# Performance work log

Measured on AMD Instinct MI355X. Metric: run time of the kernel, lower is better.

## Reference

```python
import jax, jax.numpy as jnp
import numpy as np

EPS = 1e-8


def _dtw_distance(cost):
    """Classic DTW DP: D[i,j] = cost[i,j] + min(D[i-1,j], D[i-1,j-1], D[i,j-1]).
    Rows are processed with lax.scan; the within-row left-to-right recurrence
    D[j] = min(a[j], D[j-1] + c[j]) is solved in closed form as a min-plus scan:
    with S = cumsum(c), D = cummin(a - S) + S.
    """
    # first row: only horizontal moves -> running cumsum
    d0 = jnp.cumsum(cost[0])

    def row_step(prev, c):
        # prev: D[i-1, :]  (shape [m]);  c: cost[i, :]
        prev_diag = jnp.concatenate([jnp.full((1,), jnp.inf, prev.dtype), prev[:-1]])
        a = c + jnp.minimum(prev, prev_diag)          # candidate from above / diagonal
        S = jnp.cumsum(c)
        d = jax.lax.cummin(a - S) + S                 # folds in the left-neighbor path
        return d, None

    d_last, _ = jax.lax.scan(row_step, d0, cost[1:])
    return d_last[-1]


def setup_inputs() -> dict:
    key = jax.random.key(0)
    k1, k2 = jax.random.split(key)
    N1, N2, D = 4096, 4096, 1024
    return {
        "trajectory1": jax.random.normal(k1, (N1, D), dtype=jnp.float32),
        "trajectory2": jax.random.normal(k2, (N2, D), dtype=jnp.float32),
    }


def reference(trajectory1, trajectory2):
    # cosine distance matrix: 1 - <t1_hat, t2_hat>
    t1 = trajectory1 / (jnp.linalg.norm(trajectory1, axis=-1, keepdims=True) + EPS)
    t2 = trajectory2 / (jnp.linalg.norm(trajectory2, axis=-1, keepdims=True) + EPS)
    cost = 1.0 - jnp.einsum('id,jd->ij', t1, t2)      # [N1, N2]
    distance = _dtw_distance(cost)
    similarity = 1.0 / (1.0 + distance)
    return similarity
```

## Files before the change

kernel.cpp:

```cpp
#include <hip/hip_runtime.h>
#include <hip/hip_bf16.h>
#include <stdint.h>

#define KDIM 1024
#define NROW 4096
#define NCOL 4096
#define INFV 1e30f
#define INFBITS 0x7149F2CAu
#define BM 128
#define BK 32

#define SKROWS 4160
#define DLAG   28
#define EMAX   360

typedef __bf16 bf16x8 __attribute__((ext_vector_type(8)));
typedef float f32x4 __attribute__((ext_vector_type(4)));

#define CFENCE asm volatile("" ::: "memory")

__device__ __forceinline__ unsigned short f2bf(float f) {
    __hip_bfloat16 h = __float2bfloat16(f);
    return *reinterpret_cast<unsigned short*>(&h);
}

__device__ __forceinline__ void gll16(const void* gsrc, void* ldst) {
    __builtin_amdgcn_global_load_lds(
        (const __attribute__((address_space(1))) void*)gsrc,
        (__attribute__((address_space(3))) void*)ldst, 16, 0, 0);
}

__global__ __launch_bounds__(256) void normalize_bf16(
    const float* __restrict__ t1, const float* __restrict__ t2,
    unsigned short* __restrict__ o1, unsigned short* __restrict__ o2)
{
    int b = blockIdx.x;
    int t = threadIdx.x;
    const float* src;
    unsigned short* dst;
    if (b < NROW) { src = t1 + (size_t)b * KDIM;          dst = o1 + (size_t)b * KDIM; }
    else          { src = t2 + (size_t)(b - NROW) * KDIM; dst = o2 + (size_t)(b - NROW) * KDIM; }

    float4 v = reinterpret_cast<const float4*>(src)[t];
    float ss = v.x * v.x + v.y * v.y + v.z * v.z + v.w * v.w;
    #pragma unroll
    for (int d = 32; d >= 1; d >>= 1) ss += __shfl_xor(ss, d, 64);

    __shared__ float wsum[4];
    int wave = t >> 6;
    if ((t & 63) == 0) wsum[wave] = ss;
    __syncthreads();
    float inv = 1.0f / (sqrtf(wsum[0] + wsum[1] + wsum[2] + wsum[3]) + 1e-8f);

    ushort4 o;
    o.x = f2bf(v.x * inv);
    o.y = f2bf(v.y * inv);
    o.z = f2bf(v.z * inv);
    o.w = f2bf(v.w * inv);
    reinterpret_cast<ushort4*>(dst)[t] = o;
}

__global__ __launch_bounds__(256) void gemm_cost(
    const unsigned short* __restrict__ A,
    const unsigned short* __restrict__ B,
    unsigned short* __restrict__ Cs)
{
    __shared__ __align__(16) unsigned short As[BM * BK];
    __shared__ __align__(16) unsigned short Bs[BM * BK];

    int t    = threadIdx.x;
    int lane = t & 63;
    int wave = t >> 6;
    int i0   = blockIdx.y * BM;
    int j0   = blockIdx.x * BM;

    f32x4 acc[4][4];
    f32x4 zero = {0.f, 0.f, 0.f, 0.f};
    #pragma unroll
    for (int m = 0; m < 4; ++m)
        #pragma unroll
        for (int n = 0; n < 4; ++n) acc[m][n] = zero;

    int frow = lane & 15;
    int fk   = (lane >> 4) * 8;
    int wr   = (wave >> 1) * 64;
    int wc   = (wave & 1) * 64;

    int srow = t >> 2;
    int scb  = (t & 3) * 8;

    uint4 ra0, ra1, rb0, rb1;
    {
        ra0 = *reinterpret_cast<const uint4*>(A + (size_t)(i0 + srow) * KDIM + scb);
        ra1 = *reinterpret_cast<const uint4*>(A + (size_t)(i0 + 64 + srow) * KDIM + scb);
        rb0 = *reinterpret_cast<const uint4*>(B + (size_t)(j0 + srow) * KDIM + scb);
        rb1 = *reinterpret_cast<const uint4*>(B + (size_t)(j0 + 64 + srow) * KDIM + scb);
    }

    for (int k0 = 0; k0 < KDIM; k0 += BK) {
        __syncthreads();
        *reinterpret_cast<uint4*>(As + (size_t)t * 8)         = ra0;
        *reinterpret_cast<uint4*>(As + (size_t)(256 + t) * 8) = ra1;
        *reinterpret_cast<uint4*>(Bs + (size_t)t * 8)         = rb0;
        *reinterpret_cast<uint4*>(Bs + (size_t)(256 + t) * 8) = rb1;
        __syncthreads();

        if (k0 + BK < KDIM) {
            int kn = k0 + BK;
            ra0 = *reinterpret_cast<const uint4*>(A + (size_t)(i0 + srow) * KDIM + kn + scb);
            ra1 = *reinterpret_cast<const uint4*>(A + (size_t)(i0 + 64 + srow) * KDIM + kn + scb);
            rb0 = *reinterpret_cast<const uint4*>(B + (size_t)(j0 + srow) * KDIM + kn + scb);
            rb1 = *reinterpret_cast<const uint4*>(B + (size_t)(j0 + 64 + srow) * KDIM + kn + scb);
        }

        bf16x8 af[4], bfr[4];
        #pragma unroll
        for (int m = 0; m < 4; ++m)
            af[m] = *reinterpret_cast<const bf16x8*>(As + (wr + m * 16 + frow) * BK + fk);
        #pragma unroll
        for (int n = 0; n < 4; ++n)
            bfr[n] = *reinterpret_cast<const bf16x8*>(Bs + (wc + n * 16 + frow) * BK + fk);

        #pragma unroll
        for (int m = 0; m < 4; ++m)
            #pragma unroll
            for (int n = 0; n < 4; ++n)
                acc[m][n] = __builtin_amdgcn_mfma_f32_16x16x32_bf16(af[m], bfr[n], acc[m][n], 0, 0, 0);
    }

    int crow = (lane >> 4) * 4;
    int ccol = lane & 15;
    #pragma unroll
    for (int n = 0; n < 4; ++n) {
        const int j  = j0 + wc + n * 16 + ccol;
        const int Lj = (j >> 2) & 63;
        #pragma unroll
        for (int m = 0; m < 4; ++m) {
            const int ibase = i0 + wr + m * 16 + crow;
            #pragma unroll
            for (int q = 0; q < 4; ++q)
                Cs[(size_t)(ibase + q + Lj) * NCOL + j] = f2bf(1.0f - acc[m][n][q]);
        }
    }
}

__global__ __launch_bounds__(256, 1) void dtw_systolic(
    const unsigned short* __restrict__ cost,
    unsigned long long* __restrict__ ring,
    float* __restrict__ out)
{
    __shared__ __align__(16) unsigned char clds[4 * 4 * 8192];
    __shared__ float outRow[4][128];
    __shared__ float outRowD[4][128];

    const int w    = blockIdx.x;
    const int tid  = threadIdx.x;
    const int v    = tid >> 6;
    const int lane = tid & 63;
    const int stripe = 4 * w + v;
    const bool gCon  = (v == 0 && w > 0);
    const bool gPro  = (v == 3 && w < 3);
    const bool first = (stripe == 0);
    const char* skewb = (const char*)cost;
    const unsigned long long* rseg = ring + (size_t)(w > 0 ? w - 1 : 0) * 4096;
    unsigned long long* wseg = ring + (size_t)w * 4096;
    unsigned long long* garb = ring + (size_t)3 * 4096 + w * 64;
    const unsigned lmin = (lane < 16) ? (unsigned)lane : 15u;
    const unsigned stripeByte = (unsigned)stripe * 512u + ((unsigned)(lane & 31) << 4);
    unsigned char* myclds = clds + v * 32768;
    float* opw = (lane == 63) ? outRow[v] : outRowD[v];

    float pd0 = INFV, pd1 = INFV, pd2 = INFV, pd3 = INFV;
    float lprev = (first && lane == 0) ? 0.0f : INFV;
    float d3p = INFV;
    unsigned ansb = INFBITS;
    unsigned long long rv0 = 0, rv1 = 0, rv2 = 0;

#define GLL8(STG) { int sg_ = (STG); sg_ = sg_ < 0 ? 0 : (sg_ > 259 ? 259 : sg_); \
    unsigned char* ldsb_ = myclds + (sg_ & 3) * 8192; \
    _Pragma("unroll") \
    for (int g_ = 0; g_ < 8; ++g_) { \
        int sr_ = 16 * sg_ + 2 * g_ + (lane >> 5); \
        if (sr_ > SKROWS - 1) sr_ = SKROWS - 1; \
        gll16(skewb + (size_t)sr_ * 8192 + stripeByte, ldsb_ + g_ * 1024); } }

#define RINGLD(DST, BI) { int pb_ = (BI); pb_ = pb_ < 0 ? 0 : (pb_ > 255 ? 255 : pb_); \
    const unsigned off_ = (16u * (unsigned)pb_ + lmin) * 8u; \
    asm volatile("global_load_dwordx2 %0, %1, %2 sc0 sc1" \
                 : "=v"(DST) : "v"(off_), "s"(rseg) : "memory"); }

#define DCOMP(K, CU) { \
    const unsigned rbK = (unsigned)__builtin_amdgcn_readlane(rvhi, (K)); \
    const float lcur = __uint_as_float((unsigned)__builtin_amdgcn_update_dpp( \
        (int)rbK, (int)__float_as_uint(d3p), 0x138, 0xf, 0xf, false)); \
    const float c0 = __uint_as_float(CU.x << 16); \
    const float c1 = __uint_as_float(CU.x & 0xffff0000u); \
    const float c2 = __uint_as_float(CU.y << 16); \
    const float c3 = __uint_as_float(CU.y & 0xffff0000u); \
    const float n0 = c0 + fminf(pd0, lprev); \
    const float n1 = c1 + fminf(pd1, pd0); \
    const float n2 = c2 + fminf(pd2, pd1); \
    const float n3 = c3 + fminf(pd3, pd2); \
    const float e0 = fminf(lcur + c0, n0); \
    const float e1 = fminf(e0 + c1, n1); \
    const float e2 = fminf(e1 + c2, n2); \
    const float e3 = fminf(e2 + c3, n3); \
    opw[(unsigned)(rowbase + (K)) & 127u] = e3; \
    ansb = (tjb + (K) == 4158) ? __float_as_uint(e3) : ansb; \
    lprev = lcur; d3p = e3; \
    pd0 = e0; pd1 = e1; pd2 = e2; pd3 = e3; }

    if (v == 0) {
        if (gCon) { GLL8(0) RINGLD(rv0, 0) GLL8(1) RINGLD(rv1, 1)
                    GLL8(2) RINGLD(rv2, 2) }
        else      { GLL8(0) GLL8(1) GLL8(2) }
    }

    #pragma unroll 1
    for (int e = 0; e < EMAX; ++e) {
        CFENCE;
        asm volatile("s_waitcnt lgkmcnt(0)" ::: "memory");
        __builtin_amdgcn_s_barrier();
        CFENCE;

        const int ib = e - 5 * v - DLAG * w;

        GLL8(ib + 3)
        unsigned long long rvN = 0;
        if (gCon) RINGLD(rvN, ib + 3)

        if (gCon) {
            asm volatile("s_waitcnt vmcnt(27)" : "+v"(rv0) :: "memory");
        } else if (gPro) {
            asm volatile("s_waitcnt vmcnt(27)" ::: "memory");
        } else {
            asm volatile("s_waitcnt vmcnt(24)" ::: "memory");
        }

        if (ib >= 0 && ib < 260) {
            const uint2* lu = reinterpret_cast<const uint2*>(
                myclds + (ib & 3) * 8192 + (lane << 3));
            const uint2 cc0  = lu[0 * 64],  cc1  = lu[1 * 64];
            const uint2 cc2  = lu[2 * 64],  cc3  = lu[3 * 64];
            const uint2 cc4  = lu[4 * 64],  cc5  = lu[5 * 64];
            const uint2 cc6  = lu[6 * 64],  cc7  = lu[7 * 64];
            const uint2 cc8  = lu[8 * 64],  cc9  = lu[9 * 64];
            const uint2 cc10 = lu[10 * 64], cc11 = lu[11 * 64];
            const uint2 cc12 = lu[12 * 64], cc13 = lu[13 * 64];
            const uint2 cc14 = lu[14 * 64], cc15 = lu[15 * 64];

            int rvhi;
            if (gCon) {
                if (ib < 256) {
                    const unsigned expt = 16u * (unsigned)ib + lmin + 1u;
                    while (__ballot((unsigned)rv0 == expt) != ~0ull)
                        rv0 = __hip_atomic_load(rseg + 16u * (unsigned)ib + lmin,
                                                __ATOMIC_RELAXED, __HIP_MEMORY_SCOPE_AGENT);
                }
                rvhi = (int)(unsigned)(rv0 >> 32);
            } else if (v > 0) {
                rvhi = (int)__float_as_uint(
                    outRow[v - 1][(16u * (unsigned)ib + lmin) & 127u]);
            } else {
                rvhi = (int)INFBITS;
            }

            const int rowbase = 16 * ib - 63;
            const int tjb = 16 * ib;

            DCOMP(0,  cc0)  DCOMP(1,  cc1)  DCOMP(2,  cc2)  DCOMP(3,  cc3)
            DCOMP(4,  cc4)  DCOMP(5,  cc5)  DCOMP(6,  cc6)  DCOMP(7,  cc7)
            DCOMP(8,  cc8)  DCOMP(9,  cc9)  DCOMP(10, cc10) DCOMP(11, cc11)
            DCOMP(12, cc12) DCOMP(13, cc13) DCOMP(14, cc14) DCOMP(15, cc15)
        }

        if (gPro) {
            const int r = 16 * ib - 63 + (int)lmin;
            const float bv = outRow[3][(unsigned)r & 127u];
            const bool valid = (lane < 16) && (ib >= 0) && (ib < 260) &&
                               (r >= 0) && (r <= 4095);
            if (lane < 16) {
                const unsigned long long pk =
                    ((unsigned long long)__float_as_uint(bv) << 32) | (unsigned)(r + 1);
                unsigned long long* sp = valid ? (wseg + r) : (garb + lane);
                (void)__hip_atomic_exchange(sp, pk, __ATOMIC_RELAXED,
                                            __HIP_MEMORY_SCOPE_AGENT);
            }
        }

        rv0 = rv1; rv1 = rv2; rv2 = rvN;
    }

#undef GLL8
#undef RINGLD
#undef DCOMP

    if (stripe == 15 && lane == 63) out[0] = 1.0f / (1.0f + __uint_as_float(ansb));
}

extern "C" void kernel_launch(void* const* d_in, const int* in_sizes, int n_in,
                              void* d_out, int out_size, void* d_ws, size_t ws_size,
                              hipStream_t stream)
{
    const float* t1 = (const float*)d_in[0];
    const float* t2 = (const float*)d_in[1];
    float* out = (float*)d_out;

    char* ws = (char*)d_ws;
    unsigned short* t1n  = (unsigned short*)ws;
    unsigned short* t2n  = (unsigned short*)(ws + (size_t)NROW * KDIM * 2);
    unsigned short* skew = (unsigned short*)(ws + (size_t)16 * 1024 * 1024);
    unsigned long long* ring = (unsigned long long*)(ws + (size_t)52 * 1024 * 1024);

    hipMemsetAsync(ring, 0, (size_t)(3 * 4096 + 4 * 64) * 8, stream);
    normalize_bf16<<<2 * NROW, 256, 0, stream>>>(t1, t2, t1n, t2n);
    gemm_cost<<<dim3(NCOL / BM, NROW / BM), 256, 0, stream>>>(t1n, t2n, skew);
    dtw_systolic<<<4, 256, 0, stream>>>(skew, ring, out);
}
```

Before: 644.7 us.

## Double DTW wavefront step to 32 rows and shorten prefetch pipeline

The systolic DTW kernel now processes 32 anti-diagonal rows per barrier step instead of 16. That halves the number of outer iterations, barriers and ring handoffs between workgroups. The LDS staging drops from a 4-deep ring of 16-row chunks to a 2-deep double buffer of 32-row chunks with one-ahead prefetch. Wave and block lags and the ring indexing are retuned to match. The cost is longer per-step latency, a longer inter-wave pipeline fill, and less prefetch depth to hide global-load latency.

```diff
diff --git a/kernel.cpp b/kernel.cpp
--- a/kernel.cpp
+++ b/kernel.cpp
@@ -11,8 +11,9 @@
 #define BK 32
 
 #define SKROWS 4160
-#define DLAG   28
-#define EMAX   360
+#define NBLK32 130
+#define DLAG   16
+#define EMAX   190
 
 typedef __bf16 bf16x8 __attribute__((ext_vector_type(8)));
 typedef float f32x4 __attribute__((ext_vector_type(4)));
@@ -149,9 +150,9 @@
     unsigned long long* __restrict__ ring,
     float* __restrict__ out)
 {
-    __shared__ __align__(16) unsigned char clds[4 * 4 * 8192];
+    __shared__ __align__(16) unsigned char clds[4 * 2 * 16384];
     __shared__ float outRow[4][128];
-    __shared__ float outRowD[4][128];
+    __shared__ float outRowD[4][64];
 
     const int w    = blockIdx.x;
     const int tid  = threadIdx.x;
@@ -165,27 +166,26 @@
     const unsigned long long* rseg = ring + (size_t)(w > 0 ? w - 1 : 0) * 4096;
     unsigned long long* wseg = ring + (size_t)w * 4096;
     unsigned long long* garb = ring + (size_t)3 * 4096 + w * 64;
-    const unsigned lmin = (lane < 16) ? (unsigned)lane : 15u;
+    const unsigned l32 = (unsigned)(lane & 31);
     const unsigned stripeByte = (unsigned)stripe * 512u + ((unsigned)(lane & 31) << 4);
     unsigned char* myclds = clds + v * 32768;
-    float* opw = (lane == 63) ? outRow[v] : outRowD[v];
 
     float pd0 = INFV, pd1 = INFV, pd2 = INFV, pd3 = INFV;
     float lprev = (first && lane == 0) ? 0.0f : INFV;
     float d3p = INFV;
     unsigned ansb = INFBITS;
-    unsigned long long rv0 = 0, rv1 = 0, rv2 = 0;
-
-#define GLL8(STG) { int sg_ = (STG); sg_ = sg_ < 0 ? 0 : (sg_ > 259 ? 259 : sg_); \
-    unsigned char* ldsb_ = myclds + (sg_ & 3) * 8192; \
+    unsigned long long rv0 = 0;
+
+#define GLL16S(STG) { int sg_ = (STG); sg_ = sg_ < 0 ? 0 : (sg_ > NBLK32 - 1 ? NBLK32 - 1 : sg_); \
+    unsigned char* ldsb_ = myclds + (sg_ & 1) * 16384; \
     _Pragma("unroll") \
-    for (int g_ = 0; g_ < 8; ++g_) { \
-        int sr_ = 16 * sg_ + 2 * g_ + (lane >> 5); \
+    for (int g_ = 0; g_ < 16; ++g_) { \
+        int sr_ = 32 * sg_ + 2 * g_ + (lane >> 5); \
         if (sr_ > SKROWS - 1) sr_ = SKROWS - 1; \
         gll16(skewb + (size_t)sr_ * 8192 + stripeByte, ldsb_ + g_ * 1024); } }
 
-#define RINGLD(DST, BI) { int pb_ = (BI); pb_ = pb_ < 0 ? 0 : (pb_ > 255 ? 255 : pb_); \
-    const unsigned off_ = (16u * (unsigned)pb_ + lmin) * 8u; \
+#define RINGLD(DST, BI) { int pb_ = (BI); pb_ = pb_ < 0 ? 0 : (pb_ > 127 ? 127 : pb_); \
+    const unsigned off_ = (32u * (unsigned)pb_ + l32) * 8u; \
     asm volatile("global_load_dwordx2 %0, %1, %2 sc0 sc1" \
                  : "=v"(DST) : "v"(off_), "s"(rseg) : "memory"); }
 
@@ -205,15 +205,16 @@
     const float e1 = fminf(e0 + c1, n1); \
     const float e2 = fminf(e1 + c2, n2); \
     const float e3 = fminf(e2 + c3, n3); \
-    opw[(unsigned)(rowbase + (K)) & 127u] = e3; \
+    float* sp_ = (lane == 63) ? &outRow[v][(unsigned)(rowbase + (K)) & 127u] \
+                              : &outRowD[v][lane]; \
+    *sp_ = e3; \
     ansb = (tjb + (K) == 4158) ? __float_as_uint(e3) : ansb; \
     lprev = lcur; d3p = e3; \
     pd0 = e0; pd1 = e1; pd2 = e2; pd3 = e3; }
 
     if (v == 0) {
-        if (gCon) { GLL8(0) RINGLD(rv0, 0) GLL8(1) RINGLD(rv1, 1)
-                    GLL8(2) RINGLD(rv2, 2) }
-        else      { GLL8(0) GLL8(1) GLL8(2) }
+        GLL16S(0)
+        if (gCon) RINGLD(rv0, 0)
     }
 
     #pragma unroll 1
@@ -223,23 +224,23 @@
         __builtin_amdgcn_s_barrier();
         CFENCE;
 
-        const int ib = e - 5 * v - DLAG * w;
-
-        GLL8(ib + 3)
+        const int ib = e - 3 * v - DLAG * w;
+
+        GLL16S(ib + 1)
         unsigned long long rvN = 0;
-        if (gCon) RINGLD(rvN, ib + 3)
+        if (gCon) RINGLD(rvN, ib + 1)
 
         if (gCon) {
-            asm volatile("s_waitcnt vmcnt(27)" : "+v"(rv0) :: "memory");
+            asm volatile("s_waitcnt vmcnt(17)" : "+v"(rv0) :: "memory");
         } else if (gPro) {
-            asm volatile("s_waitcnt vmcnt(27)" ::: "memory");
+            asm volatile("s_waitcnt vmcnt(17)" ::: "memory");
         } else {
-            asm volatile("s_waitcnt vmcnt(24)" ::: "memory");
-        }
-
-        if (ib >= 0 && ib < 260) {
+            asm volatile("s_waitcnt vmcnt(16)" ::: "memory");
+        }
+
+        if (ib >= 0 && ib < NBLK32) {
             const uint2* lu = reinterpret_cast<const uint2*>(
-                myclds + (ib & 3) * 8192 + (lane << 3));
+                myclds + (ib & 1) * 16384 + (lane << 3));
             const uint2 cc0  = lu[0 * 64],  cc1  = lu[1 * 64];
             const uint2 cc2  = lu[2 * 64],  cc3  = lu[3 * 64];
             const uint2 cc4  = lu[4 * 64],  cc5  = lu[5 * 64];
@@ -248,38 +249,50 @@
             const uint2 cc10 = lu[10 * 64], cc11 = lu[11 * 64];
             const uint2 cc12 = lu[12 * 64], cc13 = lu[13 * 64];
             const uint2 cc14 = lu[14 * 64], cc15 = lu[15 * 64];
+            const uint2 cc16 = lu[16 * 64], cc17 = lu[17 * 64];
+            const uint2 cc18 = lu[18 * 64], cc19 = lu[19 * 64];
+            const uint2 cc20 = lu[20 * 64], cc21 = lu[21 * 64];
+            const uint2 cc22 = lu[22 * 64], cc23 = lu[23 * 64];
+            const uint2 cc24 = lu[24 * 64], cc25 = lu[25 * 64];
+            const uint2 cc26 = lu[26 * 64], cc27 = lu[27 * 64];
+            const uint2 cc28 = lu[28 * 64], cc29 = lu[29 * 64];
+            const uint2 cc30 = lu[30 * 64], cc31 = lu[31 * 64];
 
             int rvhi;
             if (gCon) {
-                if (ib < 256) {
-                    const unsigned expt = 16u * (unsigned)ib + lmin + 1u;
+                if (ib < 128) {
+                    const unsigned expt = 32u * (unsigned)ib + l32 + 1u;
                     while (__ballot((unsigned)rv0 == expt) != ~0ull)
-                        rv0 = __hip_atomic_load(rseg + 16u * (unsigned)ib + lmin,
+                        rv0 = __hip_atomic_load(rseg + 32u * (unsigned)ib + l32,
                                                 __ATOMIC_RELAXED, __HIP_MEMORY_SCOPE_AGENT);
                 }
                 rvhi = (int)(unsigned)(rv0 >> 32);
             } else if (v > 0) {
                 rvhi = (int)__float_as_uint(
-                    outRow[v - 1][(16u * (unsigned)ib + lmin) & 127u]);
+                    outRow[v - 1][(32u * (unsigned)ib + l32) & 127u]);
             } else {
                 rvhi = (int)INFBITS;
             }
 
-            const int rowbase = 16 * ib - 63;
-            const int tjb = 16 * ib;
+            const int rowbase = 32 * ib - 63;
+            const int tjb = 32 * ib;
 
             DCOMP(0,  cc0)  DCOMP(1,  cc1)  DCOMP(2,  cc2)  DCOMP(3,  cc3)
             DCOMP(4,  cc4)  DCOMP(5,  cc5)  DCOMP(6,  cc6)  DCOMP(7,  cc7)
             DCOMP(8,  cc8)  DCOMP(9,  cc9)  DCOMP(10, cc10) DCOMP(11, cc11)
             DCOMP(12, cc12) DCOMP(13, cc13) DCOMP(14, cc14) DCOMP(15, cc15)
+            DCOMP(16, cc16) DCOMP(17, cc17) DCOMP(18, cc18) DCOMP(19, cc19)
+            DCOMP(20, cc20) DCOMP(21, cc21) DCOMP(22, cc22) DCOMP(23, cc23)
+            DCOMP(24, cc24) DCOMP(25, cc25) DCOMP(26, cc26) DCOMP(27, cc27)
+            DCOMP(28, cc28) DCOMP(29, cc29) DCOMP(30, cc30) DCOMP(31, cc31)
         }
 
         if (gPro) {
-            const int r = 16 * ib - 63 + (int)lmin;
+            const int r = 32 * ib - 63 + (int)l32;
             const float bv = outRow[3][(unsigned)r & 127u];
-            const bool valid = (lane < 16) && (ib >= 0) && (ib < 260) &&
+            const bool valid = (lane < 32) && (ib >= 0) && (ib < NBLK32) &&
                                (r >= 0) && (r <= 4095);
-            if (lane < 16) {
+            if (lane < 32) {
                 const unsigned long long pk =
                     ((unsigned long long)__float_as_uint(bv) << 32) | (unsigned)(r + 1);
                 unsigned long long* sp = valid ? (wseg + r) : (garb + lane);
@@ -288,10 +301,10 @@
             }
         }
 
-        rv0 = rv1; rv1 = rv2; rv2 = rvN;
-    }
-
-#undef GLL8
+        rv0 = rvN;
+    }
+
+#undef GLL16S
 #undef RINGLD
 #undef DCOMP
 
```

After: 600.8 us. -6.8%, faster.
